# Optimization experiments

Measured on AMD Instinct MI355X. Metric: run time of the kernel, lower is better.

The kernel has to match this reference:

```python
import jax, jax.numpy as jnp
import numpy as np

D_MODEL = 1024
NUM_HEADS = 16
D_HEAD = 64  # d_q = d_k = d_v
BATCH = 4
SEQ = 2048


def _trunc_normal(key, shape, std):
    # truncated normal in [-3*std, 3*std], matching nn.init.trunc_normal_
    return jax.random.truncated_normal(key, -3.0, 3.0, shape, dtype=jnp.float32) * std


def setup_inputs() -> dict:
    key = jax.random.key(0)
    k_x, k_q, k_k, k_v, k_o = jax.random.split(key, 5)
    hd = NUM_HEADS * D_HEAD
    s_in = np.sqrt(2.0 / (D_MODEL + hd))
    s_out = np.sqrt(2.0 / (hd + D_MODEL))
    return {
        "in_features": jax.random.normal(k_x, (BATCH, SEQ, D_MODEL), dtype=jnp.float32),
        "w_q": _trunc_normal(k_q, (hd, D_MODEL), s_in),
        "w_k": _trunc_normal(k_k, (hd, D_MODEL), s_in),
        "w_v": _trunc_normal(k_v, (hd, D_MODEL), s_in),
        "w_o": _trunc_normal(k_o, (D_MODEL, hd), s_out),
    }


def reference(in_features, w_q, w_k, w_v, w_o):
    B, S, D = in_features.shape
    H, Dh = NUM_HEADS, D_HEAD
    # QKV projections (weight stored as [out, in])
    q = jnp.einsum('od,bsd->bso', w_q, in_features).reshape(B, S, H, Dh).transpose(0, 2, 1, 3)
    k = jnp.einsum('od,bsd->bso', w_k, in_features).reshape(B, S, H, Dh).transpose(0, 2, 1, 3)
    v = jnp.einsum('od,bsd->bso', w_v, in_features).reshape(B, S, H, Dh).transpose(0, 2, 1, 3)
    # scaled dot-product attention with dense causal mask (as in source)
    att = jnp.einsum('bhqd,bhkd->bhqk', q, k) / jnp.sqrt(jnp.float32(Dh)).astype(q.dtype)
    causal = jnp.tril(jnp.ones((S, S), dtype=bool))
    att = jnp.where(causal, att, -jnp.inf)
    att = jax.nn.softmax(att, axis=-1)
    out = jnp.einsum('bhqk,bhkd->bhqd', att, v)  # [B,H,S,Dh]
    out = out.transpose(0, 2, 1, 3).reshape(B, S, H * Dh)
    return jnp.einsum('od,bsd->bso', w_o, out)
```

## Files before the change

### kernel.cpp

```cpp
#include <hip/hip_runtime.h>
#include <stdint.h>

#define D_MODEL 1024
#define NHEADS  16
#define DHEAD   64
#define BATCH   4
#define SEQ     2048
#define MTOT    (BATCH*SEQ)

typedef unsigned short u16;
typedef uint32_t u32;
typedef __bf16 bf16x8 __attribute__((ext_vector_type(8)));
typedef float  f32x4  __attribute__((ext_vector_type(4)));
typedef float  f32x16 __attribute__((ext_vector_type(16)));
typedef u16    u16x8  __attribute__((ext_vector_type(8)));
typedef u16    u16x4  __attribute__((ext_vector_type(4)));
typedef u32    u32x4  __attribute__((ext_vector_type(4)));

__device__ __forceinline__ u16 f2bf(float f) {
  uint32_t u = __builtin_bit_cast(uint32_t, f);
  u += 0x7fff + ((u >> 16) & 1);
  return (u16)(u >> 16);
}

__device__ __forceinline__ void gll16(const u16* g, u16* lds) {
  __builtin_amdgcn_global_load_lds(
      (__attribute__((address_space(1))) void*)(g),
      (__attribute__((address_space(3))) void*)(lds), 16, 0, 0);
}

__global__ void cvtk(const float4* __restrict__ in, u16x4* __restrict__ out, int n4) {
  const int i = blockIdx.x * blockDim.x + threadIdx.x;
  if (i < n4) {
    const float4 f = in[i];
    u16x4 h;
    h[0] = f2bf(f.x); h[1] = f2bf(f.y); h[2] = f2bf(f.z); h[3] = f2bf(f.w);
    out[i] = h;
  }
}

template<int MODE>
__launch_bounds__(256)
__global__ void gemm_bt_k(const u16* __restrict__ A,
                          const u16* __restrict__ W0,
                          const u16* __restrict__ W1,
                          const u16* __restrict__ W2,
                          void* __restrict__ Cout)
{
  constexpr int K = D_MODEL;
  const int tid = threadIdx.x;
  const int l = tid & 63, w = tid >> 6;
  const int m0 = blockIdx.x * 128;
  const int n0 = blockIdx.y * 128;
  const u16* Bm = W0;
  float scale = 1.0f;
  if (MODE == 1) {
    const int z = blockIdx.z;
    Bm = (z == 0) ? W0 : ((z == 1) ? W1 : W2);
    scale = (z == 0) ? 0.125f * 1.44269504088896f : 1.0f;
  }

  __shared__ __align__(16) u16 As[128*32];
  __shared__ __align__(16) u16 Bs[128*32];

  f32x4 acc[4][4];
  #pragma unroll
  for (int i = 0; i < 4; ++i)
    #pragma unroll
    for (int j = 0; j < 4; ++j)
      acc[i][j] = f32x4{0.f, 0.f, 0.f, 0.f};

  const int wr = w >> 1, wc = w & 1;
  const int srow = l >> 2;
  const int scol = (l & 3) * 8;

  for (int k0 = 0; k0 < K; k0 += 32) {
    __syncthreads();
    #pragma unroll
    for (int j = 0; j < 2; ++j) {
      const int seg = w * 2 + j;
      gll16(A  + (size_t)(m0 + seg*16 + srow) * K + k0 + scol, &As[seg*512]);
      gll16(Bm + (size_t)(n0 + seg*16 + srow) * K + k0 + scol, &Bs[seg*512]);
    }
    __syncthreads();
    bf16x8 af[4], bfr[4];
    #pragma unroll
    for (int m = 0; m < 4; ++m)
      af[m] = *(const bf16x8*)&As[(wr*64 + m*16 + (l & 15))*32 + (l >> 4)*8];
    #pragma unroll
    for (int n = 0; n < 4; ++n)
      bfr[n] = *(const bf16x8*)&Bs[(wc*64 + n*16 + (l & 15))*32 + (l >> 4)*8];
    #pragma unroll
    for (int m = 0; m < 4; ++m)
      #pragma unroll
      for (int n = 0; n < 4; ++n)
        acc[m][n] = __builtin_amdgcn_mfma_f32_16x16x32_bf16(af[m], bfr[n], acc[m][n], 0, 0, 0);
  }

  const int g = l >> 4, c15 = l & 15;
  #pragma unroll
  for (int m = 0; m < 4; ++m) {
    #pragma unroll
    for (int n = 0; n < 4; ++n) {
      #pragma unroll
      for (int j = 0; j < 4; ++j) {
        const int row = m0 + wr*64 + m*16 + g*4 + j;
        const int col = n0 + wc*64 + n*16 + c15;
        const float v = acc[m][n][j] * scale;
        if (MODE == 0) {
          ((float*)Cout)[(size_t)row * D_MODEL + col] = v;
        } else {
          const int b = row >> 11, s = row & (SEQ-1);
          const int h = col >> 6, dh = col & (DHEAD-1);
          ((u16*)Cout)[(size_t)blockIdx.z * MTOT * D_MODEL
                       + ((size_t)(b*NHEADS + h) * SEQ + s) * DHEAD + dh] = f2bf(v);
        }
      }
    }
  }
}

__launch_bounds__(512)
__global__ void attn3_k(const u16* __restrict__ Qb, const u16* __restrict__ Kb_,
                        const u16* __restrict__ Vb_, u16* __restrict__ Oa)
{
  const int tid = threadIdx.x;
  const int w = tid >> 6, l = tid & 63;
  const int q5 = l & 31, hi = l >> 5;
  const int r = blockIdx.x;
  const int bh = (r & 7) * 8 + ((r >> 3) & 7);
  const int pairi = r >> 6;
  const int b = bh >> 4, h = bh & 15;
  const size_t base = (size_t)bh * SEQ * DHEAD;
  const u16* Qg = Qb + base;
  const u16* Kg = Kb_ + base;
  const u16* Vg = Vb_ + base;

  __shared__ __align__(16) u16 smem[16384];

  const int kc = tid & 7, row = tid >> 3;
  const int kr8 = l >> 3;
  const int kkv = 8*w + kr8;
  const int kdc = (l & 7) ^ kr8 ^ w;

  int vidx[8];
  #pragma unroll
  for (int e = 0; e < 8; ++e)
    vidx[e] = (8*kc + e)*64 + (((row >> 3) ^ kc ^ e) & 7)*8 + (row & 7);

  for (int half = 0; half < 2; ++half) {
    const int tq = half ? (7 - pairi) : pairi;
    const int q0w = tq*256 + 32*w;
    const int ntk = (tq + 1) * 4;
    const int ntw = (q0w >> 6) + 1;

    bf16x8 qf[4];
    #pragma unroll
    for (int s = 0; s < 4; ++s)
      qf[s] = *(const bf16x8*)(Qg + (size_t)(q0w + q5)*DHEAD + 16*s + 8*hi);

    f32x16 c0 = {}, c1 = {};
    float mrun = -1e30f, lrun = 0.f;

    {
      gll16(Kg + (size_t)kkv*DHEAD + kdc*8, smem + w*512);
      const u16x8 vr0 = *(const u16x8*)(Vg + (size_t)row*DHEAD + kc*8);
      #pragma unroll
      for (int e = 0; e < 8; ++e) smem[8192 + vidx[e]] = vr0[e];
    }
    __syncthreads();

    for (int t = 0; t < ntk; ++t) {
      const int cur = t & 1;
      const bool pf = (t + 1 < ntk);
      u16x8 vr;
      if (pf) {
        vr = *(const u16x8*)(Vg + (size_t)((t+1)*64 + row)*DHEAD + kc*8);
        gll16(Kg + (size_t)((t+1)*64 + kkv)*DHEAD + kdc*8,
              smem + (cur^1)*4096 + w*512);
      }

      if (t < ntw) {
        const u16* Kb = smem + cur*4096;
        const u16* Vv = smem + 8192 + cur*4096;

        f32x16 st[2] = {{}, {}};
        __builtin_amdgcn_s_setprio(1);
        #pragma unroll
        for (int kb = 0; kb < 2; ++kb) {
          #pragma unroll
          for (int s = 0; s < 4; ++s) {
            const int slot = ((2*s + hi) ^ (l & 7) ^ (4*kb) ^ (q5 >> 3)) & 7;
            const bf16x8 kf = *(const bf16x8*)(Kb + (32*kb + q5)*64 + slot*8);
            st[kb] = __builtin_amdgcn_mfma_f32_32x32x16_bf16(kf, qf[s], st[kb], 0, 0, 0);
          }
        }
        __builtin_amdgcn_s_setprio(0);

        if (t == ntw - 1) {
          const int kv0 = t*64;
          #pragma unroll
          for (int kb = 0; kb < 2; ++kb)
            #pragma unroll
            for (int rr = 0; rr < 16; ++rr) {
              const int kvg = kv0 + 32*kb + (rr & 3) + 8*(rr >> 2) + 4*hi;
              if (kvg > q0w + q5) st[kb][rr] = -1e30f;
            }
        }

        float mx = -1e30f;
        #pragma unroll
        for (int kb = 0; kb < 2; ++kb)
          #pragma unroll
          for (int rr = 0; rr < 16; ++rr) mx = fmaxf(mx, st[kb][rr]);
        mx = fmaxf(mx, __shfl_xor(mx, 32));
        const float mnew = fmaxf(mrun, mx);
        const float alpha = __builtin_amdgcn_exp2f(mrun - mnew);
        mrun = mnew;
        float rs = 0.f;
        #pragma unroll
        for (int kb = 0; kb < 2; ++kb)
          #pragma unroll
          for (int rr = 0; rr < 16; ++rr) {
            const float p = __builtin_amdgcn_exp2f(st[kb][rr] - mnew);
            st[kb][rr] = p;
            rs += p;
          }
        rs += __shfl_xor(rs, 32);
        lrun = lrun * alpha + rs;
        #pragma unroll
        for (int rr = 0; rr < 16; ++rr) { c0[rr] *= alpha; c1[rr] *= alpha; }

        bf16x8 pb[4];
        #pragma unroll
        for (int kb = 0; kb < 2; ++kb) {
          u32 pw[8];
          #pragma unroll
          for (int i = 0; i < 8; ++i) {
            u32 t0;
            asm("v_cvt_pk_bf16_f32 %0, %1, %2"
                : "=v"(t0) : "v"(st[kb][2*i]), "v"(st[kb][2*i+1]));
            pw[i] = t0;
          }
          asm("v_permlane32_swap_b32 %0, %1" : "+v"(pw[0]), "+v"(pw[2]));
          asm("v_permlane32_swap_b32 %0, %1" : "+v"(pw[1]), "+v"(pw[3]));
          asm("v_permlane32_swap_b32 %0, %1" : "+v"(pw[4]), "+v"(pw[6]));
          asm("v_permlane32_swap_b32 %0, %1" : "+v"(pw[5]), "+v"(pw[7]));
          pb[2*kb]   = __builtin_bit_cast(bf16x8, u32x4{pw[0], pw[1], pw[2], pw[3]});
          pb[2*kb+1] = __builtin_bit_cast(bf16x8, u32x4{pw[4], pw[5], pw[6], pw[7]});
        }

        __builtin_amdgcn_s_setprio(1);
        #pragma unroll
        for (int s = 0; s < 4; ++s) {
          {
            const int slot = ((2*s + hi) ^ (l & 7) ^ (q5 >> 3)) & 7;
            const bf16x8 vf = *(const bf16x8*)(Vv + q5*64 + slot*8);
            c0 = __builtin_amdgcn_mfma_f32_32x32x16_bf16(vf, pb[s], c0, 0, 0, 0);
          }
          {
            const int slot = ((2*s + hi) ^ (l & 7) ^ 4 ^ (q5 >> 3)) & 7;
            const bf16x8 vf = *(const bf16x8*)(Vv + (32 + q5)*64 + slot*8);
            c1 = __builtin_amdgcn_mfma_f32_32x32x16_bf16(vf, pb[s], c1, 0, 0, 0);
          }
        }
        __builtin_amdgcn_s_setprio(0);
      }

      if (pf) {
        u16* Vd = smem + 8192 + (cur^1)*4096;
        #pragma unroll
        for (int e = 0; e < 8; ++e) Vd[vidx[e]] = vr[e];
      }
      __syncthreads();
    }

    const float linv = __builtin_amdgcn_rcpf(lrun);
    #pragma unroll
    for (int Ab = 0; Ab < 2; ++Ab)
      #pragma unroll
      for (int rr = 0; rr < 16; ++rr) {
        const int d = 32*Ab + (rr & 3) + 8*(rr >> 2) + 4*hi;
        smem[w*2048 + q5*64 + (((d >> 3) ^ (q5 & 7)) & 7)*8 + (d & 7)] =
            f2bf((Ab ? c1[rr] : c0[rr]) * linv);
      }
    __syncthreads();
    #pragma unroll
    for (int cc = 0; cc < 4; ++cc) {
      const int dchunk = 4*hi + cc;
      const u16x8 vv = *(const u16x8*)&smem[w*2048 + q5*64 + ((dchunk ^ (q5 & 7)) & 7)*8];
      *(u16x8*)(Oa + (size_t)(b*SEQ + q0w + q5)*D_MODEL + h*DHEAD + 32*hi + 8*cc) = vv;
    }
    __syncthreads();
  }
}

extern "C" void kernel_launch(void* const* d_in, const int* in_sizes, int n_in,
                              void* d_out, int out_size, void* d_ws, size_t ws_size,
                              hipStream_t stream) {
  const float* X  = (const float*)d_in[0];
  const float* Wq = (const float*)d_in[1];
  const float* Wk = (const float*)d_in[2];
  const float* Wv = (const float*)d_in[3];
  const float* Wo = (const float*)d_in[4];

  u16* xb  = (u16*)d_ws;
  u16* wqb = xb  + (size_t)MTOT*D_MODEL;
  u16* wkb = wqb + (size_t)D_MODEL*D_MODEL;
  u16* wvb = wkb + (size_t)D_MODEL*D_MODEL;
  u16* wob = wvb + (size_t)D_MODEL*D_MODEL;
  u16* qkv = wob + (size_t)D_MODEL*D_MODEL;
  u16* att = qkv + (size_t)3*MTOT*D_MODEL;

  const int nx4 = MTOT*D_MODEL/4;
  const int nw4 = D_MODEL*D_MODEL/4;
  cvtk<<<nx4/256, 256, 0, stream>>>((const float4*)X,  (u16x4*)xb,  nx4);
  cvtk<<<nw4/256, 256, 0, stream>>>((const float4*)Wq, (u16x4*)wqb, nw4);
  cvtk<<<nw4/256, 256, 0, stream>>>((const float4*)Wk, (u16x4*)wkb, nw4);
  cvtk<<<nw4/256, 256, 0, stream>>>((const float4*)Wv, (u16x4*)wvb, nw4);
  cvtk<<<nw4/256, 256, 0, stream>>>((const float4*)Wo, (u16x4*)wob, nw4);

  dim3 g1(MTOT/128, D_MODEL/128, 3);
  gemm_bt_k<1><<<g1, 256, 0, stream>>>(xb, wqb, wkb, wvb, (void*)qkv);

  attn3_k<<<256, 512, 0, stream>>>(qkv, qkv + (size_t)MTOT*D_MODEL,
                                   qkv + (size_t)2*MTOT*D_MODEL, att);

  dim3 g3(MTOT/128, D_MODEL/128, 1);
  gemm_bt_k<0><<<g3, 256, 0, stream>>>(att, wob, nullptr, nullptr, d_out);
}
```

Baseline: 173.1 us.

## Split attention into one q-tile per block, lazy softmax rescale, batch weight casts

The attention kernel now launches 512 blocks with one 256-row query tile each, instead of 256 blocks that each processed a pair of tiles sequentially. Blocks are ordered so the heaviest causal tiles are scheduled first, aiming for better load balance and more concurrency across CUs. The online softmax now skips the max update and accumulator rescale when the new max stays within a threshold of 8 of the running max, which removes a per-tile multiply pass but leaves exponents unnormalised by up to 2^8. The four weight conversions are merged into a single launch to cut launch overhead.

```diff
diff --git a/kernel.cpp b/kernel.cpp
--- a/kernel.cpp
+++ b/kernel.cpp
@@ -37,6 +37,19 @@
     h[0] = f2bf(f.x); h[1] = f2bf(f.y); h[2] = f2bf(f.z); h[3] = f2bf(f.w);
     out[i] = h;
   }
+}
+
+__global__ void cvtk4(const float4* __restrict__ a, const float4* __restrict__ b,
+                      const float4* __restrict__ c, const float4* __restrict__ d,
+                      u16x4* __restrict__ out, int n4) {
+  const int i = blockIdx.x * blockDim.x + threadIdx.x;
+  if (i >= n4) return;
+  const float4* src = (blockIdx.y == 0) ? a : (blockIdx.y == 1) ? b
+                    : (blockIdx.y == 2) ? c : d;
+  const float4 f = src[i];
+  u16x4 h;
+  h[0] = f2bf(f.x); h[1] = f2bf(f.y); h[2] = f2bf(f.z); h[3] = f2bf(f.w);
+  out[(size_t)blockIdx.y * n4 + i] = h;
 }
 
 template<int MODE>
@@ -121,7 +134,7 @@
 }
 
 __launch_bounds__(512)
-__global__ void attn3_k(const u16* __restrict__ Qb, const u16* __restrict__ Kb_,
+__global__ void attn5_k(const u16* __restrict__ Qb, const u16* __restrict__ Kb_,
                         const u16* __restrict__ Vb_, u16* __restrict__ Oa)
 {
   const int tid = threadIdx.x;
@@ -129,7 +142,8 @@
   const int q5 = l & 31, hi = l >> 5;
   const int r = blockIdx.x;
   const int bh = (r & 7) * 8 + ((r >> 3) & 7);
-  const int pairi = r >> 6;
+  const int p = r >> 6;
+  const int tq = (p < 4) ? (7 - p) : (p - 4);
   const int b = bh >> 4, h = bh & 15;
   const size_t base = (size_t)bh * SEQ * DHEAD;
   const u16* Qg = Qb + base;
@@ -148,150 +162,149 @@
   for (int e = 0; e < 8; ++e)
     vidx[e] = (8*kc + e)*64 + (((row >> 3) ^ kc ^ e) & 7)*8 + (row & 7);
 
-  for (int half = 0; half < 2; ++half) {
-    const int tq = half ? (7 - pairi) : pairi;
-    const int q0w = tq*256 + 32*w;
-    const int ntk = (tq + 1) * 4;
-    const int ntw = (q0w >> 6) + 1;
-
-    bf16x8 qf[4];
-    #pragma unroll
-    for (int s = 0; s < 4; ++s)
-      qf[s] = *(const bf16x8*)(Qg + (size_t)(q0w + q5)*DHEAD + 16*s + 8*hi);
-
-    f32x16 c0 = {}, c1 = {};
-    float mrun = -1e30f, lrun = 0.f;
-
-    {
-      gll16(Kg + (size_t)kkv*DHEAD + kdc*8, smem + w*512);
-      const u16x8 vr0 = *(const u16x8*)(Vg + (size_t)row*DHEAD + kc*8);
-      #pragma unroll
-      for (int e = 0; e < 8; ++e) smem[8192 + vidx[e]] = vr0[e];
-    }
-    __syncthreads();
-
-    for (int t = 0; t < ntk; ++t) {
-      const int cur = t & 1;
-      const bool pf = (t + 1 < ntk);
-      u16x8 vr;
-      if (pf) {
-        vr = *(const u16x8*)(Vg + (size_t)((t+1)*64 + row)*DHEAD + kc*8);
-        gll16(Kg + (size_t)((t+1)*64 + kkv)*DHEAD + kdc*8,
-              smem + (cur^1)*4096 + w*512);
-      }
-
-      if (t < ntw) {
-        const u16* Kb = smem + cur*4096;
-        const u16* Vv = smem + 8192 + cur*4096;
-
-        f32x16 st[2] = {{}, {}};
-        __builtin_amdgcn_s_setprio(1);
-        #pragma unroll
-        for (int kb = 0; kb < 2; ++kb) {
-          #pragma unroll
-          for (int s = 0; s < 4; ++s) {
-            const int slot = ((2*s + hi) ^ (l & 7) ^ (4*kb) ^ (q5 >> 3)) & 7;
-            const bf16x8 kf = *(const bf16x8*)(Kb + (32*kb + q5)*64 + slot*8);
-            st[kb] = __builtin_amdgcn_mfma_f32_32x32x16_bf16(kf, qf[s], st[kb], 0, 0, 0);
-          }
-        }
-        __builtin_amdgcn_s_setprio(0);
-
-        if (t == ntw - 1) {
-          const int kv0 = t*64;
-          #pragma unroll
-          for (int kb = 0; kb < 2; ++kb)
-            #pragma unroll
-            for (int rr = 0; rr < 16; ++rr) {
-              const int kvg = kv0 + 32*kb + (rr & 3) + 8*(rr >> 2) + 4*hi;
-              if (kvg > q0w + q5) st[kb][rr] = -1e30f;
-            }
-        }
-
-        float mx = -1e30f;
-        #pragma unroll
-        for (int kb = 0; kb < 2; ++kb)
-          #pragma unroll
-          for (int rr = 0; rr < 16; ++rr) mx = fmaxf(mx, st[kb][rr]);
-        mx = fmaxf(mx, __shfl_xor(mx, 32));
-        const float mnew = fmaxf(mrun, mx);
-        const float alpha = __builtin_amdgcn_exp2f(mrun - mnew);
-        mrun = mnew;
-        float rs = 0.f;
+  const int q0w = tq*256 + 32*w;
+  const int ntk = (tq + 1) * 4;
+  const int ntw = (q0w >> 6) + 1;
+
+  bf16x8 qf[4];
+  #pragma unroll
+  for (int s = 0; s < 4; ++s)
+    qf[s] = *(const bf16x8*)(Qg + (size_t)(q0w + q5)*DHEAD + 16*s + 8*hi);
+
+  f32x16 c0 = {}, c1 = {};
+  float mrun = -1e30f, lrun = 0.f;
+
+  {
+    gll16(Kg + (size_t)kkv*DHEAD + kdc*8, smem + w*512);
+    const u16x8 vr0 = *(const u16x8*)(Vg + (size_t)row*DHEAD + kc*8);
+    #pragma unroll
+    for (int e = 0; e < 8; ++e) smem[8192 + vidx[e]] = vr0[e];
+  }
+  __syncthreads();
+
+  for (int t = 0; t < ntk; ++t) {
+    const int cur = t & 1;
+    const bool pf = (t + 1 < ntk);
+    u16x8 vr;
+    if (pf) {
+      vr = *(const u16x8*)(Vg + (size_t)((t+1)*64 + row)*DHEAD + kc*8);
+      gll16(Kg + (size_t)((t+1)*64 + kkv)*DHEAD + kdc*8,
+            smem + (cur^1)*4096 + w*512);
+    }
+
+    if (t < ntw) {
+      const u16* Kb = smem + cur*4096;
+      const u16* Vv = smem + 8192 + cur*4096;
+
+      f32x16 st[2] = {{}, {}};
+      __builtin_amdgcn_s_setprio(1);
+      #pragma unroll
+      for (int kb = 0; kb < 2; ++kb) {
+        #pragma unroll
+        for (int s = 0; s < 4; ++s) {
+          const int slot = ((2*s + hi) ^ (l & 7) ^ (4*kb) ^ (q5 >> 3)) & 7;
+          const bf16x8 kf = *(const bf16x8*)(Kb + (32*kb + q5)*64 + slot*8);
+          st[kb] = __builtin_amdgcn_mfma_f32_32x32x16_bf16(kf, qf[s], st[kb], 0, 0, 0);
+        }
+      }
+      __builtin_amdgcn_s_setprio(0);
+
+      if (t == ntw - 1) {
+        const int kv0 = t*64;
         #pragma unroll
         for (int kb = 0; kb < 2; ++kb)
           #pragma unroll
           for (int rr = 0; rr < 16; ++rr) {
-            const float p = __builtin_amdgcn_exp2f(st[kb][rr] - mnew);
-            st[kb][rr] = p;
-            rs += p;
+            const int kvg = kv0 + 32*kb + (rr & 3) + 8*(rr >> 2) + 4*hi;
+            if (kvg > q0w + q5) st[kb][rr] = -1e30f;
           }
-        rs += __shfl_xor(rs, 32);
-        lrun = lrun * alpha + rs;
+      }
+
+      float mx = -1e30f;
+      #pragma unroll
+      for (int kb = 0; kb < 2; ++kb)
+        #pragma unroll
+        for (int rr = 0; rr < 16; ++rr) mx = fmaxf(mx, st[kb][rr]);
+      mx = fmaxf(mx, __shfl_xor(mx, 32));
+      float alpha = 1.0f;
+      if (!__all(mx <= mrun + 8.0f)) {
+        const float mnew = fmaxf(mrun, mx);
+        alpha = __builtin_amdgcn_exp2f(mrun - mnew);
+        mrun = mnew;
         #pragma unroll
         for (int rr = 0; rr < 16; ++rr) { c0[rr] *= alpha; c1[rr] *= alpha; }
-
-        bf16x8 pb[4];
-        #pragma unroll
-        for (int kb = 0; kb < 2; ++kb) {
-          u32 pw[8];
-          #pragma unroll
-          for (int i = 0; i < 8; ++i) {
-            u32 t0;
-            asm("v_cvt_pk_bf16_f32 %0, %1, %2"
-                : "=v"(t0) : "v"(st[kb][2*i]), "v"(st[kb][2*i+1]));
-            pw[i] = t0;
-          }
-          asm("v_permlane32_swap_b32 %0, %1" : "+v"(pw[0]), "+v"(pw[2]));
-          asm("v_permlane32_swap_b32 %0, %1" : "+v"(pw[1]), "+v"(pw[3]));
-          asm("v_permlane32_swap_b32 %0, %1" : "+v"(pw[4]), "+v"(pw[6]));
-          asm("v_permlane32_swap_b32 %0, %1" : "+v"(pw[5]), "+v"(pw[7]));
-          pb[2*kb]   = __builtin_bit_cast(bf16x8, u32x4{pw[0], pw[1], pw[2], pw[3]});
-          pb[2*kb+1] = __builtin_bit_cast(bf16x8, u32x4{pw[4], pw[5], pw[6], pw[7]});
-        }
-
-        __builtin_amdgcn_s_setprio(1);
-        #pragma unroll
-        for (int s = 0; s < 4; ++s) {
-          {
-            const int slot = ((2*s + hi) ^ (l & 7) ^ (q5 >> 3)) & 7;
-            const bf16x8 vf = *(const bf16x8*)(Vv + q5*64 + slot*8);
-            c0 = __builtin_amdgcn_mfma_f32_32x32x16_bf16(vf, pb[s], c0, 0, 0, 0);
-          }
-          {
-            const int slot = ((2*s + hi) ^ (l & 7) ^ 4 ^ (q5 >> 3)) & 7;
-            const bf16x8 vf = *(const bf16x8*)(Vv + (32 + q5)*64 + slot*8);
-            c1 = __builtin_amdgcn_mfma_f32_32x32x16_bf16(vf, pb[s], c1, 0, 0, 0);
-          }
-        }
-        __builtin_amdgcn_s_setprio(0);
-      }
-
-      if (pf) {
-        u16* Vd = smem + 8192 + (cur^1)*4096;
-        #pragma unroll
-        for (int e = 0; e < 8; ++e) Vd[vidx[e]] = vr[e];
-      }
-      __syncthreads();
-    }
-
-    const float linv = __builtin_amdgcn_rcpf(lrun);
-    #pragma unroll
-    for (int Ab = 0; Ab < 2; ++Ab)
-      #pragma unroll
-      for (int rr = 0; rr < 16; ++rr) {
-        const int d = 32*Ab + (rr & 3) + 8*(rr >> 2) + 4*hi;
-        smem[w*2048 + q5*64 + (((d >> 3) ^ (q5 & 7)) & 7)*8 + (d & 7)] =
-            f2bf((Ab ? c1[rr] : c0[rr]) * linv);
-      }
+      }
+      float rs = 0.f;
+      #pragma unroll
+      for (int kb = 0; kb < 2; ++kb)
+        #pragma unroll
+        for (int rr = 0; rr < 16; ++rr) {
+          const float pe = __builtin_amdgcn_exp2f(st[kb][rr] - mrun);
+          st[kb][rr] = pe;
+          rs += pe;
+        }
+      rs += __shfl_xor(rs, 32);
+      lrun = lrun * alpha + rs;
+
+      bf16x8 pb[4];
+      #pragma unroll
+      for (int kb = 0; kb < 2; ++kb) {
+        u32 pw[8];
+        #pragma unroll
+        for (int i = 0; i < 8; ++i) {
+          u32 t0;
+          asm("v_cvt_pk_bf16_f32 %0, %1, %2"
+              : "=v"(t0) : "v"(st[kb][2*i]), "v"(st[kb][2*i+1]));
+          pw[i] = t0;
+        }
+        asm("v_permlane32_swap_b32 %0, %1" : "+v"(pw[0]), "+v"(pw[2]));
+        asm("v_permlane32_swap_b32 %0, %1" : "+v"(pw[1]), "+v"(pw[3]));
+        asm("v_permlane32_swap_b32 %0, %1" : "+v"(pw[4]), "+v"(pw[6]));
+        asm("v_permlane32_swap_b32 %0, %1" : "+v"(pw[5]), "+v"(pw[7]));
+        pb[2*kb]   = __builtin_bit_cast(bf16x8, u32x4{pw[0], pw[1], pw[2], pw[3]});
+        pb[2*kb+1] = __builtin_bit_cast(bf16x8, u32x4{pw[4], pw[5], pw[6], pw[7]});
+      }
+
+      __builtin_amdgcn_s_setprio(1);
+      #pragma unroll
+      for (int s = 0; s < 4; ++s) {
+        {
+          const int slot = ((2*s + hi) ^ (l & 7) ^ (q5 >> 3)) & 7;
+          const bf16x8 vf = *(const bf16x8*)(Vv + q5*64 + slot*8);
+          c0 = __builtin_amdgcn_mfma_f32_32x32x16_bf16(vf, pb[s], c0, 0, 0, 0);
+        }
+        {
+          const int slot = ((2*s + hi) ^ (l & 7) ^ 4 ^ (q5 >> 3)) & 7;
+          const bf16x8 vf = *(const bf16x8*)(Vv + (32 + q5)*64 + slot*8);
+          c1 = __builtin_amdgcn_mfma_f32_32x32x16_bf16(vf, pb[s], c1, 0, 0, 0);
+        }
+      }
+      __builtin_amdgcn_s_setprio(0);
+    }
+
+    if (pf) {
+      u16* Vd = smem + 8192 + (cur^1)*4096;
+      #pragma unroll
+      for (int e = 0; e < 8; ++e) Vd[vidx[e]] = vr[e];
+    }
     __syncthreads();
-    #pragma unroll
-    for (int cc = 0; cc < 4; ++cc) {
-      const int dchunk = 4*hi + cc;
-      const u16x8 vv = *(const u16x8*)&smem[w*2048 + q5*64 + ((dchunk ^ (q5 & 7)) & 7)*8];
-      *(u16x8*)(Oa + (size_t)(b*SEQ + q0w + q5)*D_MODEL + h*DHEAD + 32*hi + 8*cc) = vv;
-    }
-    __syncthreads();
+  }
+
+  const float linv = __builtin_amdgcn_rcpf(lrun);
+  #pragma unroll
+  for (int Ab = 0; Ab < 2; ++Ab)
+    #pragma unroll
+    for (int rr = 0; rr < 16; ++rr) {
+      const int d = 32*Ab + (rr & 3) + 8*(rr >> 2) + 4*hi;
+      smem[w*2048 + q5*64 + (((d >> 3) ^ (q5 & 7)) & 7)*8 + (d & 7)] =
+          f2bf((Ab ? c1[rr] : c0[rr]) * linv);
+    }
+  __syncthreads();
+  #pragma unroll
+  for (int cc = 0; cc < 4; ++cc) {
+    const int dchunk = 4*hi + cc;
+    const u16x8 vv = *(const u16x8*)&smem[w*2048 + q5*64 + ((dchunk ^ (q5 & 7)) & 7)*8];
+    *(u16x8*)(Oa + (size_t)(b*SEQ + q0w + q5)*D_MODEL + h*DHEAD + 32*hi + 8*cc) = vv;
   }
 }
 
@@ -314,16 +327,16 @@
 
   const int nx4 = MTOT*D_MODEL/4;
   const int nw4 = D_MODEL*D_MODEL/4;
-  cvtk<<<nx4/256, 256, 0, stream>>>((const float4*)X,  (u16x4*)xb,  nx4);
-  cvtk<<<nw4/256, 256, 0, stream>>>((const float4*)Wq, (u16x4*)wqb, nw4);
-  cvtk<<<nw4/256, 256, 0, stream>>>((const float4*)Wk, (u16x4*)wkb, nw4);
-  cvtk<<<nw4/256, 256, 0, stream>>>((const float4*)Wv, (u16x4*)wvb, nw4);
-  cvtk<<<nw4/256, 256, 0, stream>>>((const float4*)Wo, (u16x4*)wob, nw4);
+  cvtk<<<nx4/256, 256, 0, stream>>>((const float4*)X, (u16x4*)xb, nx4);
+  dim3 gc(nw4/256, 4, 1);
+  cvtk4<<<gc, 256, 0, stream>>>((const float4*)Wq, (const float4*)Wk,
+                                (const float4*)Wv, (const float4*)Wo,
+                                (u16x4*)wqb, nw4);
 
   dim3 g1(MTOT/128, D_MODEL/128, 3);
   gemm_bt_k<1><<<g1, 256, 0, stream>>>(xb, wqb, wkb, wvb, (void*)qkv);
 
-  attn3_k<<<256, 512, 0, stream>>>(qkv, qkv + (size_t)MTOT*D_MODEL,
+  attn5_k<<<512, 512, 0, stream>>>(qkv, qkv + (size_t)MTOT*D_MODEL,
                                    qkv + (size_t)2*MTOT*D_MODEL, att);
 
   dim3 g3(MTOT/128, D_MODEL/128, 1);
```

Result: slower. 178.5 us (+3.1%).
